# Kernel optimization log

Measured on AMD Instinct MI355X. Metric: run time of the kernel, lower is better.

Reference implementation:

```python
import jax, jax.numpy as jnp
import numpy as np

B, S, T, H, E, V, PAD = 128, 400, 50, 512, 128, 50000, 1000


def setup_inputs() -> dict:
    key = jax.random.key(0)
    ks = jax.random.split(key, 20)
    inp = {
        "input_token": jax.random.randint(ks[0], (B, 1), 0, V),
        "prev_decoder_h_states": jax.random.normal(ks[1], (B, T, H), jnp.float32),
        "last_hidden": jax.random.normal(ks[2], (B, H), jnp.float32),
        "encoder_states": jax.random.normal(ks[3], (B, S, H), jnp.float32),
        "full_input_var": jax.random.randint(ks[4], (B, S), 0, V + PAD),
        "previous_att": jax.random.normal(ks[5], (B, T, S), jnp.float32),
        "control_var": jax.random.normal(ks[6], (B, 1), jnp.float32),
        # learned parameters
        "emb": jax.random.normal(ks[7], (V, E), jnp.float32) * 0.02,
        "W_ih": jax.random.normal(ks[8], (3 * H, E), jnp.float32) * 0.05,
        "W_hh": jax.random.normal(ks[9], (3 * H, H), jnp.float32) * 0.05,
        "b_ih": jnp.zeros((3 * H,), jnp.float32),
        "b_hh": jnp.zeros((3 * H,), jnp.float32),
        "w_h": jax.random.normal(ks[10], (H,), jnp.float32) * 0.05,
        "w_d": jax.random.normal(ks[11], (H,), jnp.float32) * 0.05,
        "gen_W": jax.random.normal(ks[12], (1, 3 * H + 1), jnp.float32) * 0.05,
        "gen_b": jnp.zeros((1,), jnp.float32),
        "outh_W": jax.random.normal(ks[13], (E, 3 * H + 1), jnp.float32) * 0.05,
        "outh_b": jnp.zeros((E,), jnp.float32),
        "outv_W": jax.random.normal(ks[14], (V, E), jnp.float32) * 0.02,
        "outv_b": jnp.zeros((V,), jnp.float32),
    }
    return inp


def reference(input_token, prev_decoder_h_states, last_hidden, encoder_states,
              full_input_var, previous_att, control_var,
              emb, W_ih, W_hh, b_ih, b_hh, w_h, w_d,
              gen_W, gen_b, outh_W, outh_b, outv_W, outv_b):
    # embedding lookup (dropout = eval-mode identity); seq len is 1
    x = emb[input_token[:, 0]]                              # [B,E]
    # single GRU step (torch gate order: r, z, n)
    gx = x @ W_ih.T + b_ih                                  # [B,3H]
    gh = last_hidden @ W_hh.T + b_hh                        # [B,3H]
    r = jax.nn.sigmoid(gx[:, :H] + gh[:, :H])
    z = jax.nn.sigmoid(gx[:, H:2 * H] + gh[:, H:2 * H])
    n = jnp.tanh(gx[:, 2 * H:] + r * gh[:, 2 * H:])
    h = (1.0 - z) * n + z * last_hidden                     # decoder_hidden [B,H]

    # temporal encoder attention (previous_att is not None branch)
    att_scores = jnp.einsum("bh,bsh->bs", h, w_h[None, None, :] * encoder_states)
    temporal = jnp.exp(att_scores) / jnp.exp(previous_att).sum(1)   # [B,S]
    new_previous_att = jnp.concatenate([previous_att, att_scores[:, None, :]], axis=1)
    att_dist = temporal / temporal.sum(-1, keepdims=True)           # [B,S]

    # intra-decoder attention
    dec_scores = jnp.einsum("bh,bth->bt", h, w_d[None, None, :] * prev_decoder_h_states)
    dec_att = jax.nn.softmax(dec_scores, axis=-1)                   # [B,T]
    decoder_context = jnp.einsum("bt,bth->bh", dec_att, prev_decoder_h_states)

    encoder_context = jnp.einsum("bs,bsh->bh", att_dist, encoder_states)
    combined = jnp.concatenate([h, encoder_context, decoder_context, control_var], axis=-1)  # [B,3H+1]

    p_vocab = jax.nn.softmax((combined @ outh_W.T + outh_b) @ outv_W.T + outv_b, axis=-1)    # [B,V]
    p_gen = jax.nn.sigmoid(combined @ gen_W.T + gen_b)                                       # [B,1]

    # copy distribution via scatter-add over extended vocab V+PAD
    token_input_dist = jnp.zeros((input_token.shape[0], V + PAD), p_vocab.dtype)
    rows = jnp.arange(input_token.shape[0])[:, None]
    token_input_dist = token_input_dist.at[rows, full_input_var].add(att_dist)

    p_final = jnp.pad(p_vocab * p_gen, ((0, 0), (0, PAD))) + (1.0 - p_gen) * token_input_dist
    decoder_h_states = jnp.concatenate([prev_decoder_h_states, h[:, None, :]], axis=1)
    return (p_final, p_gen, p_vocab, att_dist, decoder_h_states, h, new_previous_att)
```

## Files before the change

kernel.cpp:

```cpp
#include <hip/hip_runtime.h>
#include <hip/hip_bf16.h>
#include <math.h>

constexpr int B = 128, S = 400, T = 50, H = 512, E = 128, V = 50000, PADV = 1000;
constexpr int NV = V + PADV;
constexpr int TH1 = 3 * H + 1;
constexpr int NBLK = 391;

constexpr int O_PFINAL = 0;
constexpr int O_PGEN   = O_PFINAL + B * NV;
constexpr int O_PVOCAB = O_PGEN + B;
constexpr int O_ATT    = O_PVOCAB + B * V;
constexpr int O_DHS    = O_ATT + B * S;
constexpr int O_H      = O_DHS + B * (T + 1) * H;
constexpr int O_NPA    = O_H + B * H;

constexpr int W_X    = 0;
constexpr int W_GX   = W_X + B * E;
constexpr int W_GH   = W_GX + B * 3 * H;
constexpr int W_HW   = W_GH + B * 3 * H;
constexpr int W_HD   = W_HW + B * H;
constexpr int W_SC   = W_HD + B * H;
constexpr int W_DEN  = W_SC + B * S;
constexpr int W_CMB  = W_DEN + B * S;
constexpr int W_LE   = W_CMB + B * TH1;
constexpr int W_RMAX = W_LE + B * E;
constexpr int W_RSUM = W_RMAX + B;
constexpr int W_PM   = W_RSUM + B;
constexpr int W_PS   = W_PM + B * NBLK;

__device__ __forceinline__ float wave_sum(float v) {
#pragma unroll
  for (int o = 32; o > 0; o >>= 1) v += __shfl_xor(v, o);
  return v;
}

__global__ void k_init(const int* __restrict__ tok, const float* __restrict__ emb,
                       const float* __restrict__ ctrl, float* __restrict__ ws) {
  int i = blockIdx.x * 256 + threadIdx.x;
  if (i < B * E) {
    int b = i >> 7, e = i & 127;
    ws[W_X + i] = emb[tok[b] * E + e];
  }
  if (i < B * H) {
    int b = i >> 9, h = i & 511;
    ws[W_CMB + b * TH1 + H + h] = 0.f;
  }
  if (i < B) ws[W_CMB + i * TH1 + 3 * H] = ctrl[i];
#pragma unroll
  for (int j = 0; j < 3; ++j) ws[W_GH + i + j * 65536] = 0.f;
}

__global__ __launch_bounds__(256) void k_grugemm(
    const float* __restrict__ x, const float* __restrict__ lh,
    const float* __restrict__ Wih, const float* __restrict__ Whh,
    float* __restrict__ ws) {
  __shared__ float As[32][132];
  __shared__ float Ws[32][36];
  const int tid = threadIdx.x;
  const int n0 = blockIdx.x * 32;
  const int y = blockIdx.y;
  const bool g0 = (y == 0);
  const float* A = g0 ? x : lh;
  const float* W = g0 ? Wih : Whh;
  const int K = g0 ? E : H;
  const int kbase = g0 ? 0 : (y - 1) * 128;
  const int tc = tid & 15;
  const int tr = tid >> 4;
  float acc[8][2] = {};
  for (int c = 0; c < 4; ++c) {
    const int k0 = kbase + c * 32;
    {
      int i = tid;
#pragma unroll
      for (int it = 0; it < 4; ++it, i += 256) {
        int b = i >> 3, k4 = i & 7;
        float4 v = *(const float4*)&A[b * K + k0 + k4 * 4];
        As[k4 * 4 + 0][b] = v.x; As[k4 * 4 + 1][b] = v.y;
        As[k4 * 4 + 2][b] = v.z; As[k4 * 4 + 3][b] = v.w;
      }
    }
    {
      int n = tid >> 3, k4 = tid & 7;
      float4 v = *(const float4*)&W[(n0 + n) * K + k0 + k4 * 4];
      Ws[k4 * 4 + 0][n] = v.x; Ws[k4 * 4 + 1][n] = v.y;
      Ws[k4 * 4 + 2][n] = v.z; Ws[k4 * 4 + 3][n] = v.w;
    }
    __syncthreads();
#pragma unroll
    for (int kk = 0; kk < 32; ++kk) {
      float4 a0 = *(const float4*)&As[kk][tr * 8];
      float4 a1 = *(const float4*)&As[kk][tr * 8 + 4];
      float2 w = *(const float2*)&Ws[kk][tc * 2];
      float av[8] = {a0.x, a0.y, a0.z, a0.w, a1.x, a1.y, a1.z, a1.w};
#pragma unroll
      for (int i = 0; i < 8; ++i) {
        acc[i][0] += av[i] * w.x;
        acc[i][1] += av[i] * w.y;
      }
    }
    __syncthreads();
  }
  if (g0) {
#pragma unroll
    for (int i = 0; i < 8; ++i) {
      float* dst = ws + W_GX + (tr * 8 + i) * (3 * H) + n0 + tc * 2;
      dst[0] = acc[i][0]; dst[1] = acc[i][1];
    }
  } else {
#pragma unroll
    for (int i = 0; i < 8; ++i) {
      float* dst = ws + W_GH + (tr * 8 + i) * (3 * H) + n0 + tc * 2;
      atomicAdd(dst, acc[i][0]); atomicAdd(dst + 1, acc[i][1]);
    }
  }
}

__global__ void k_gates(const float* __restrict__ ws_in, const float* __restrict__ lh,
                        const float* __restrict__ bih, const float* __restrict__ bhh,
                        const float* __restrict__ w_h, const float* __restrict__ w_d,
                        float* __restrict__ ws, float* __restrict__ out) {
  int i = blockIdx.x * 256 + threadIdx.x;
  int b = i >> 9, u = i & 511;
  const float* gx = ws_in + W_GX + b * (3 * H);
  const float* gh = ws_in + W_GH + b * (3 * H);
  float gxr = gx[u] + bih[u], gxz = gx[H + u] + bih[H + u], gxn = gx[2 * H + u] + bih[2 * H + u];
  float ghr = gh[u] + bhh[u], ghz = gh[H + u] + bhh[H + u], ghn = gh[2 * H + u] + bhh[2 * H + u];
  float r = 1.f / (1.f + __expf(-(gxr + ghr)));
  float z = 1.f / (1.f + __expf(-(gxz + ghz)));
  float n = tanhf(gxn + r * ghn);
  float lhv = lh[i];
  float h = (1.f - z) * n + z * lhv;
  out[O_H + i] = h;
  out[O_DHS + b * ((T + 1) * H) + T * H + u] = h;
  ws[W_CMB + b * TH1 + u] = h;
  ws[W_HW + i] = h * w_h[u];
  ws[W_HD + i] = h * w_d[u];
}

__global__ void k_den(const float* __restrict__ pa, float* __restrict__ ws,
                      float* __restrict__ out) {
  int i = blockIdx.x * 256 + threadIdx.x;
  if (i >= B * S) return;
  int b = i / S, s = i - b * S;
  float acc = 0.f;
  for (int t = 0; t < T; ++t) {
    float v = pa[(b * T + t) * S + s];
    out[O_NPA + (b * (T + 1) + t) * S + s] = v;
    acc += __expf(v);
  }
  ws[W_DEN + i] = acc;
}

__global__ void k_escore(const float* __restrict__ enc, float* __restrict__ ws,
                         float* __restrict__ out) {
  int blk = blockIdx.x;
  int b = blk / 25, sgrp = blk % 25;
  int wave = threadIdx.x >> 6, lane = threadIdx.x & 63;
  const float4* hw4 = (const float4*)(ws + W_HW + b * H);
  float4 h0 = hw4[lane * 2], h1 = hw4[lane * 2 + 1];
#pragma unroll
  for (int ii = 0; ii < 4; ++ii) {
    int s = sgrp * 16 + wave * 4 + ii;
    const float4* e4 = (const float4*)(enc + (b * S + s) * H);
    float4 e0 = e4[lane * 2], e1 = e4[lane * 2 + 1];
    float d = h0.x * e0.x + h0.y * e0.y + h0.z * e0.z + h0.w * e0.w +
              h1.x * e1.x + h1.y * e1.y + h1.z * e1.z + h1.w * e1.w;
    d = wave_sum(d);
    if (lane == 0) {
      ws[W_SC + b * S + s] = d;
      out[O_NPA + (b * (T + 1) + T) * S + s] = d;
    }
  }
}

__global__ void k_attdist(const float* __restrict__ ws, float* __restrict__ out) {
  int b = blockIdx.x, tid = threadIdx.x;
  __shared__ float red[4];
  int s0 = tid, s1 = tid + 256;
  float t0 = __expf(ws[W_SC + b * S + s0]) / ws[W_DEN + b * S + s0];
  float t1 = 0.f;
  if (s1 < S) t1 = __expf(ws[W_SC + b * S + s1]) / ws[W_DEN + b * S + s1];
  float loc = wave_sum(t0 + t1);
  if ((tid & 63) == 0) red[tid >> 6] = loc;
  __syncthreads();
  float inv = 1.f / (red[0] + red[1] + red[2] + red[3]);
  out[O_ATT + b * S + s0] = t0 * inv;
  if (s1 < S) out[O_ATT + b * S + s1] = t1 * inv;
}

__global__ void k_dec(const float* __restrict__ pd, float* __restrict__ ws,
                      float* __restrict__ out) {
  int b = blockIdx.x, tid = threadIdx.x;
  int wave = tid >> 6, lane = tid & 63;
  __shared__ float sc[T];
  const float4* hd4 = (const float4*)(ws + W_HD + b * H);
  float4 d0 = hd4[lane * 2], d1 = hd4[lane * 2 + 1];
  for (int t = wave; t < T; t += 4) {
    const float4* p4 = (const float4*)(pd + (b * T + t) * H);
    float4 p0 = p4[lane * 2], p1 = p4[lane * 2 + 1];
    float v = d0.x * p0.x + d0.y * p0.y + d0.z * p0.z + d0.w * p0.w +
              d1.x * p1.x + d1.y * p1.y + d1.z * p1.z + d1.w * p1.w;
    v = wave_sum(v);
    if (lane == 0) sc[t] = v;
  }
  __syncthreads();
  if (tid < 64) {
    float v = (lane < T) ? sc[lane] : -1e30f;
    float m = v;
#pragma unroll
    for (int o = 32; o > 0; o >>= 1) m = fmaxf(m, __shfl_xor(m, o));
    float e = (lane < T) ? __expf(v - m) : 0.f;
    float ssum = wave_sum(e);
    if (lane < T) sc[lane] = e / ssum;
  }
  __syncthreads();
  float a0 = 0.f, a1 = 0.f;
  int h0 = tid, h1 = tid + 256;
  for (int t = 0; t < T; ++t) {
    float wt = sc[t];
    a0 += wt * pd[(b * T + t) * H + h0];
    a1 += wt * pd[(b * T + t) * H + h1];
  }
  ws[W_CMB + b * TH1 + 2 * H + h0] = a0;
  ws[W_CMB + b * TH1 + 2 * H + h1] = a1;
}

__global__ void k_dhscopy(const float* __restrict__ pd, float* __restrict__ out) {
  int i = blockIdx.x * 256 + threadIdx.x;
  if (i >= B * T * H / 4) return;
  int b = i / (T * H / 4), rem = i - b * (T * H / 4);
  ((float4*)(out + O_DHS + b * (T + 1) * H))[rem] = ((const float4*)(pd + b * T * H))[rem];
}

__global__ void k_encctx(const float* __restrict__ enc, const float* __restrict__ out,
                         float* __restrict__ ws) {
  int blk = blockIdx.x;
  int b = blk / 5, c = blk % 5;
  int s0 = c * 80, tid = threadIdx.x;
  __shared__ float ad[80];
  if (tid < 80) ad[tid] = out[O_ATT + b * S + s0 + tid];
  __syncthreads();
  float a0 = 0.f, a1 = 0.f;
  int h0 = tid, h1 = tid + 256;
  for (int j = 0; j < 80; ++j) {
    float w = ad[j];
    const float* ep = enc + (b * S + s0 + j) * H;
    a0 += w * ep[h0];
    a1 += w * ep[h1];
  }
  atomicAdd(&ws[W_CMB + b * TH1 + H + h0], a0);
  atomicAdd(&ws[W_CMB + b * TH1 + H + h1], a1);
}

__global__ __launch_bounds__(256) void k_outh2(const float* __restrict__ oW,
                                               const float* __restrict__ ob,
                                               float* __restrict__ ws) {
  __shared__ float cmb[8 * TH1];
  const int tid = threadIdx.x;
  const int b0 = blockIdx.y * 8;
  const int e = blockIdx.x * 4 + (tid >> 6);
  const int lane = tid & 63;
  const float* src = ws + W_CMB + b0 * TH1;
  for (int i = tid; i < 8 * TH1; i += 256) cmb[i] = src[i];
  float wr[25];
  const float* wrow = oW + e * TH1;
#pragma unroll
  for (int j = 0; j < 25; ++j) {
    int k = lane + 64 * j;
    wr[j] = (k < TH1) ? wrow[k] : 0.f;
  }
  __syncthreads();
  float bias = ob[e];
#pragma unroll 1
  for (int bb = 0; bb < 8; ++bb) {
    const float* c = cmb + bb * TH1;
    float a = 0.f;
#pragma unroll
    for (int j = 0; j < 25; ++j) {
      int k = lane + 64 * j;
      float cv = (k < TH1) ? c[k] : 0.f;
      a += wr[j] * cv;
    }
    a = wave_sum(a);
    if (lane == 0) ws[W_LE + (b0 + bb) * E + e] = a + bias;
  }
}

__global__ void k_gen(const float* __restrict__ gW, const float* __restrict__ gb,
                      const float* __restrict__ ws, float* __restrict__ out) {
  int b = blockIdx.x, lane = threadIdx.x;
  float acc = 0.f;
  for (int k = lane; k < TH1; k += 64) acc += gW[k] * ws[W_CMB + b * TH1 + k];
  acc = wave_sum(acc);
  if (lane == 0) out[O_PGEN + b] = 1.f / (1.f + __expf(-(acc + gb[0])));
}

__global__ __launch_bounds__(256) void k_vgemm(
    const float* __restrict__ A, const float* __restrict__ W,
    const float* __restrict__ bias, float* __restrict__ C,
    float* __restrict__ ws) {
  __shared__ float As[32][132];
  __shared__ float Bs[32][132];
  const int tid = threadIdx.x;
  const int n0 = blockIdx.x * 128;
  const int tr = tid >> 4;
  const int tc = tid & 15;
  float acc[8][8] = {};
#pragma unroll 1
  for (int c = 0; c < 4; ++c) {
    const int k0 = c * 32;
    {
      int i = tid;
#pragma unroll
      for (int it = 0; it < 4; ++it, i += 256) {
        int m = i >> 3, k4 = i & 7;
        float4 v = *(const float4*)&A[m * 128 + k0 + k4 * 4];
        As[k4 * 4 + 0][m] = v.x; As[k4 * 4 + 1][m] = v.y;
        As[k4 * 4 + 2][m] = v.z; As[k4 * 4 + 3][m] = v.w;
      }
    }
    {
      int i = tid;
#pragma unroll
      for (int it = 0; it < 4; ++it, i += 256) {
        int n = i >> 3, k4 = i & 7;
        float4 v = make_float4(0.f, 0.f, 0.f, 0.f);
        if (n0 + n < V) v = *(const float4*)&W[(n0 + n) * 128 + k0 + k4 * 4];
        Bs[k4 * 4 + 0][n] = v.x; Bs[k4 * 4 + 1][n] = v.y;
        Bs[k4 * 4 + 2][n] = v.z; Bs[k4 * 4 + 3][n] = v.w;
      }
    }
    __syncthreads();
#pragma unroll 4
    for (int kk = 0; kk < 32; ++kk) {
      float4 a0 = *(const float4*)&As[kk][tr * 8];
      float4 a1 = *(const float4*)&As[kk][tr * 8 + 4];
      float4 b0 = *(const float4*)&Bs[kk][tc * 8];
      float4 b1 = *(const float4*)&Bs[kk][tc * 8 + 4];
      float av[8] = {a0.x, a0.y, a0.z, a0.w, a1.x, a1.y, a1.z, a1.w};
      float bw[8] = {b0.x, b0.y, b0.z, b0.w, b1.x, b1.y, b1.z, b1.w};
#pragma unroll
      for (int i = 0; i < 8; ++i)
#pragma unroll
        for (int j = 0; j < 8; ++j) acc[i][j] += av[i] * bw[j];
    }
    __syncthreads();
  }
  const int cbase = n0 + tc * 8;
  float bv[8];
#pragma unroll
  for (int j = 0; j < 8; ++j) bv[j] = (cbase + j < V) ? bias[cbase + j] : 0.f;
#pragma unroll
  for (int i = 0; i < 8; ++i) {
    int r = tr * 8 + i;
    float m = -1e30f;
#pragma unroll
    for (int j = 0; j < 8; ++j) {
      acc[i][j] += bv[j];
      if (cbase + j < V) m = fmaxf(m, acc[i][j]);
    }
#pragma unroll
    for (int o = 1; o < 16; o <<= 1) m = fmaxf(m, __shfl_xor(m, o));
    float s = 0.f;
#pragma unroll
    for (int j = 0; j < 8; ++j)
      if (cbase + j < V) s += __expf(acc[i][j] - m);
#pragma unroll
    for (int o = 1; o < 16; o <<= 1) s += __shfl_xor(s, o);
    if (tc == 0) {
      ws[W_PM + r * NBLK + blockIdx.x] = m;
      ws[W_PS + r * NBLK + blockIdx.x] = s;
    }
    if (cbase + 8 <= V) {
      *(float4*)&C[r * V + cbase] = make_float4(acc[i][0], acc[i][1], acc[i][2], acc[i][3]);
      *(float4*)&C[r * V + cbase + 4] = make_float4(acc[i][4], acc[i][5], acc[i][6], acc[i][7]);
    } else {
#pragma unroll
      for (int j = 0; j < 8; ++j)
        if (cbase + j < V) C[r * V + cbase + j] = acc[i][j];
    }
  }
}

__global__ void k_rowstat2(float* __restrict__ ws) {
  int b = blockIdx.x, tid = threadIdx.x;
  const float* pm = ws + W_PM + b * NBLK;
  const float* psv = ws + W_PS + b * NBLK;
  __shared__ float red[4];
  float m = -1e30f;
  for (int c = tid; c < NBLK; c += 256) m = fmaxf(m, pm[c]);
#pragma unroll
  for (int o = 32; o > 0; o >>= 1) m = fmaxf(m, __shfl_xor(m, o));
  if ((tid & 63) == 0) red[tid >> 6] = m;
  __syncthreads();
  float M = fmaxf(fmaxf(red[0], red[1]), fmaxf(red[2], red[3]));
  __syncthreads();
  float s = 0.f;
  for (int c = tid; c < NBLK; c += 256) s += psv[c] * __expf(pm[c] - M);
  s = wave_sum(s);
  if ((tid & 63) == 0) red[tid >> 6] = s;
  __syncthreads();
  if (tid == 0) {
    ws[W_RMAX + b] = M;
    ws[W_RSUM + b] = red[0] + red[1] + red[2] + red[3];
  }
}

__global__ void k_pvocab(const float* __restrict__ ws, float* __restrict__ out) {
  int b = blockIdx.y;
  int i = blockIdx.x * 256 + threadIdx.x;
  if (i >= V / 4) return;
  float m = ws[W_RMAX + b], inv = 1.f / ws[W_RSUM + b];
  float pg = out[O_PGEN + b];
  float4 v = ((const float4*)(out + O_PVOCAB + b * V))[i];
  float4 p;
  p.x = __expf(v.x - m) * inv;
  p.y = __expf(v.y - m) * inv;
  p.z = __expf(v.z - m) * inv;
  p.w = __expf(v.w - m) * inv;
  ((float4*)(out + O_PVOCAB + b * V))[i] = p;
  float4 pf;
  pf.x = pg * p.x; pf.y = pg * p.y; pf.z = pg * p.z; pf.w = pg * p.w;
  ((float4*)(out + O_PFINAL + b * NV))[i] = pf;
}

__global__ void k_pad(float* __restrict__ out) {
  int i = blockIdx.x * 256 + threadIdx.x;
  if (i >= B * PADV / 4) return;
  int b = i / (PADV / 4), j = i % (PADV / 4);
  ((float4*)(out + O_PFINAL + b * NV + V))[j] = make_float4(0.f, 0.f, 0.f, 0.f);
}

__global__ void k_scatter(const int* __restrict__ fiv, float* __restrict__ out) {
  int i = blockIdx.x * 256 + threadIdx.x;
  if (i >= B * S) return;
  int b = i / S;
  int idx = fiv[i];
  float pg = out[O_PGEN + b];
  float val = (1.f - pg) * out[O_ATT + i];
  atomicAdd(out + O_PFINAL + b * NV + idx, val);
}

extern "C" void kernel_launch(void* const* d_in, const int* in_sizes, int n_in,
                              void* d_out, int out_size, void* d_ws, size_t ws_size,
                              hipStream_t stream) {
  const int*   tok  = (const int*)d_in[0];
  const float* pd   = (const float*)d_in[1];
  const float* lh   = (const float*)d_in[2];
  const float* enc  = (const float*)d_in[3];
  const int*   fiv  = (const int*)d_in[4];
  const float* pa   = (const float*)d_in[5];
  const float* ctrl = (const float*)d_in[6];
  const float* emb  = (const float*)d_in[7];
  const float* W_ih = (const float*)d_in[8];
  const float* W_hh = (const float*)d_in[9];
  const float* b_ih = (const float*)d_in[10];
  const float* b_hh = (const float*)d_in[11];
  const float* w_h  = (const float*)d_in[12];
  const float* w_d  = (const float*)d_in[13];
  const float* gW   = (const float*)d_in[14];
  const float* gb   = (const float*)d_in[15];
  const float* ohW  = (const float*)d_in[16];
  const float* ohb  = (const float*)d_in[17];
  const float* ovW  = (const float*)d_in[18];
  const float* ovb  = (const float*)d_in[19];
  float* out = (float*)d_out;
  float* ws  = (float*)d_ws;

  k_init<<<256, 256, 0, stream>>>(tok, emb, ctrl, ws);
  k_grugemm<<<dim3(48, 5), 256, 0, stream>>>(ws + W_X, lh, W_ih, W_hh, ws);
  k_gates<<<256, 256, 0, stream>>>(ws, lh, b_ih, b_hh, w_h, w_d, ws, out);
  k_den<<<200, 256, 0, stream>>>(pa, ws, out);
  k_escore<<<3200, 256, 0, stream>>>(enc, ws, out);
  k_attdist<<<128, 256, 0, stream>>>(ws, out);
  k_dec<<<128, 256, 0, stream>>>(pd, ws, out);
  k_dhscopy<<<3200, 256, 0, stream>>>(pd, out);
  k_encctx<<<640, 256, 0, stream>>>(enc, out, ws);
  k_outh2<<<dim3(32, 16), 256, 0, stream>>>(ohW, ohb, ws);
  k_gen<<<128, 64, 0, stream>>>(gW, gb, ws, out);
  k_vgemm<<<NBLK, 256, 0, stream>>>(ws + W_LE, ovW, ovb, out + O_PVOCAB, ws);
  k_rowstat2<<<128, 256, 0, stream>>>(ws);
  k_pvocab<<<dim3(49, 128), 256, 0, stream>>>(ws, out);
  k_pad<<<125, 256, 0, stream>>>(out);
  k_scatter<<<200, 256, 0, stream>>>(fiv, out);
}
```

Before: 386.7 us.

## Fuse encoder context into score kernel and fold pad zeroing into pvocab

The encoder-score kernel now also computes the unnormalised attention weights exp(score)/den and accumulates a weighted sum of the encoder rows it already holds in registers. It also accumulates the per-batch weight total, both through atomics. This removes the separate k_encctx pass that re-read the whole 26 MB encoder tensor. The attdist kernel then normalises both the attention and the context by the accumulated total. Pad zeroing moves into k_pvocab as an extra grid column, dropping one launch. The cost is more atomic traffic and a change in float summation order.

```diff
diff --git a/kernel.cpp b/kernel.cpp
--- a/kernel.cpp
+++ b/kernel.cpp
@@ -28,6 +28,8 @@
 constexpr int W_RSUM = W_RMAX + B;
 constexpr int W_PM   = W_RSUM + B;
 constexpr int W_PS   = W_PM + B * NBLK;
+constexpr int W_ECX  = W_PS + B * NBLK;
+constexpr int W_TS   = W_ECX + B * H;
 
 __device__ __forceinline__ float wave_sum(float v) {
 #pragma unroll
@@ -42,11 +44,11 @@
     int b = i >> 7, e = i & 127;
     ws[W_X + i] = emb[tok[b] * E + e];
   }
-  if (i < B * H) {
-    int b = i >> 9, h = i & 511;
-    ws[W_CMB + b * TH1 + H + h] = 0.f;
-  }
-  if (i < B) ws[W_CMB + i * TH1 + 3 * H] = ctrl[i];
+  ws[W_ECX + i] = 0.f;
+  if (i < B) {
+    ws[W_TS + i] = 0.f;
+    ws[W_CMB + i * TH1 + 3 * H] = ctrl[i];
+  }
 #pragma unroll
   for (int j = 0; j < 3; ++j) ws[W_GH + i + j * 65536] = 0.f;
 }
@@ -154,11 +156,16 @@
 
 __global__ void k_escore(const float* __restrict__ enc, float* __restrict__ ws,
                          float* __restrict__ out) {
+  __shared__ float ctx[4][512];
+  __shared__ float tsw[4];
   int blk = blockIdx.x;
   int b = blk / 25, sgrp = blk % 25;
-  int wave = threadIdx.x >> 6, lane = threadIdx.x & 63;
+  int tid = threadIdx.x;
+  int wave = tid >> 6, lane = tid & 63;
   const float4* hw4 = (const float4*)(ws + W_HW + b * H);
   float4 h0 = hw4[lane * 2], h1 = hw4[lane * 2 + 1];
+  float c0[4] = {}, c1[4] = {};
+  float tsum = 0.f;
 #pragma unroll
   for (int ii = 0; ii < 4; ++ii) {
     int s = sgrp * 16 + wave * 4 + ii;
@@ -167,26 +174,35 @@
     float d = h0.x * e0.x + h0.y * e0.y + h0.z * e0.z + h0.w * e0.w +
               h1.x * e1.x + h1.y * e1.y + h1.z * e1.z + h1.w * e1.w;
     d = wave_sum(d);
+    float tmp = __expf(d) / ws[W_DEN + b * S + s];
     if (lane == 0) {
-      ws[W_SC + b * S + s] = d;
+      ws[W_SC + b * S + s] = tmp;
       out[O_NPA + (b * (T + 1) + T) * S + s] = d;
     }
-  }
-}
-
-__global__ void k_attdist(const float* __restrict__ ws, float* __restrict__ out) {
+    tsum += tmp;
+    c0[0] += tmp * e0.x; c0[1] += tmp * e0.y; c0[2] += tmp * e0.z; c0[3] += tmp * e0.w;
+    c1[0] += tmp * e1.x; c1[1] += tmp * e1.y; c1[2] += tmp * e1.z; c1[3] += tmp * e1.w;
+  }
+  *(float4*)&ctx[wave][lane * 8]     = make_float4(c0[0], c0[1], c0[2], c0[3]);
+  *(float4*)&ctx[wave][lane * 8 + 4] = make_float4(c1[0], c1[1], c1[2], c1[3]);
+  if (lane == 0) tsw[wave] = tsum;
+  __syncthreads();
+  for (int h = tid; h < H; h += 256) {
+    float v = ctx[0][h] + ctx[1][h] + ctx[2][h] + ctx[3][h];
+    atomicAdd(&ws[W_ECX + b * H + h], v);
+  }
+  if (tid == 0) atomicAdd(&ws[W_TS + b], tsw[0] + tsw[1] + tsw[2] + tsw[3]);
+}
+
+__global__ void k_attdist(const float* __restrict__ ws_in, float* __restrict__ ws,
+                          float* __restrict__ out) {
   int b = blockIdx.x, tid = threadIdx.x;
-  __shared__ float red[4];
+  float inv = 1.f / ws_in[W_TS + b];
   int s0 = tid, s1 = tid + 256;
-  float t0 = __expf(ws[W_SC + b * S + s0]) / ws[W_DEN + b * S + s0];
-  float t1 = 0.f;
-  if (s1 < S) t1 = __expf(ws[W_SC + b * S + s1]) / ws[W_DEN + b * S + s1];
-  float loc = wave_sum(t0 + t1);
-  if ((tid & 63) == 0) red[tid >> 6] = loc;
-  __syncthreads();
-  float inv = 1.f / (red[0] + red[1] + red[2] + red[3]);
-  out[O_ATT + b * S + s0] = t0 * inv;
-  if (s1 < S) out[O_ATT + b * S + s1] = t1 * inv;
+  out[O_ATT + b * S + s0] = ws_in[W_SC + b * S + s0] * inv;
+  if (s1 < S) out[O_ATT + b * S + s1] = ws_in[W_SC + b * S + s1] * inv;
+  for (int h = tid; h < H; h += 256)
+    ws[W_CMB + b * TH1 + H + h] = ws_in[W_ECX + b * H + h] * inv;
 }
 
 __global__ void k_dec(const float* __restrict__ pd, float* __restrict__ ws,
@@ -231,26 +247,6 @@
   if (i >= B * T * H / 4) return;
   int b = i / (T * H / 4), rem = i - b * (T * H / 4);
   ((float4*)(out + O_DHS + b * (T + 1) * H))[rem] = ((const float4*)(pd + b * T * H))[rem];
-}
-
-__global__ void k_encctx(const float* __restrict__ enc, const float* __restrict__ out,
-                         float* __restrict__ ws) {
-  int blk = blockIdx.x;
-  int b = blk / 5, c = blk % 5;
-  int s0 = c * 80, tid = threadIdx.x;
-  __shared__ float ad[80];
-  if (tid < 80) ad[tid] = out[O_ATT + b * S + s0 + tid];
-  __syncthreads();
-  float a0 = 0.f, a1 = 0.f;
-  int h0 = tid, h1 = tid + 256;
-  for (int j = 0; j < 80; ++j) {
-    float w = ad[j];
-    const float* ep = enc + (b * S + s0 + j) * H;
-    a0 += w * ep[h0];
-    a1 += w * ep[h1];
-  }
-  atomicAdd(&ws[W_CMB + b * TH1 + H + h0], a0);
-  atomicAdd(&ws[W_CMB + b * TH1 + H + h1], a1);
 }
 
 __global__ __launch_bounds__(256) void k_outh2(const float* __restrict__ oW,
@@ -410,7 +406,11 @@
 __global__ void k_pvocab(const float* __restrict__ ws, float* __restrict__ out) {
   int b = blockIdx.y;
   int i = blockIdx.x * 256 + threadIdx.x;
-  if (i >= V / 4) return;
+  if (i >= NV / 4) return;
+  if (i >= V / 4) {
+    ((float4*)(out + O_PFINAL + b * NV))[i] = make_float4(0.f, 0.f, 0.f, 0.f);
+    return;
+  }
   float m = ws[W_RMAX + b], inv = 1.f / ws[W_RSUM + b];
   float pg = out[O_PGEN + b];
   float4 v = ((const float4*)(out + O_PVOCAB + b * V))[i];
@@ -423,13 +423,6 @@
   float4 pf;
   pf.x = pg * p.x; pf.y = pg * p.y; pf.z = pg * p.z; pf.w = pg * p.w;
   ((float4*)(out + O_PFINAL + b * NV))[i] = pf;
-}
-
-__global__ void k_pad(float* __restrict__ out) {
-  int i = blockIdx.x * 256 + threadIdx.x;
-  if (i >= B * PADV / 4) return;
-  int b = i / (PADV / 4), j = i % (PADV / 4);
-  ((float4*)(out + O_PFINAL + b * NV + V))[j] = make_float4(0.f, 0.f, 0.f, 0.f);
 }
 
 __global__ void k_scatter(const int* __restrict__ fiv, float* __restrict__ out) {
@@ -473,15 +466,13 @@
   k_gates<<<256, 256, 0, stream>>>(ws, lh, b_ih, b_hh, w_h, w_d, ws, out);
   k_den<<<200, 256, 0, stream>>>(pa, ws, out);
   k_escore<<<3200, 256, 0, stream>>>(enc, ws, out);
-  k_attdist<<<128, 256, 0, stream>>>(ws, out);
+  k_attdist<<<128, 256, 0, stream>>>(ws, ws, out);
   k_dec<<<128, 256, 0, stream>>>(pd, ws, out);
   k_dhscopy<<<3200, 256, 0, stream>>>(pd, out);
-  k_encctx<<<640, 256, 0, stream>>>(enc, out, ws);
   k_outh2<<<dim3(32, 16), 256, 0, stream>>>(ohW, ohb, ws);
   k_gen<<<128, 64, 0, stream>>>(gW, gb, ws, out);
   k_vgemm<<<NBLK, 256, 0, stream>>>(ws + W_LE, ovW, ovb, out + O_PVOCAB, ws);
   k_rowstat2<<<128, 256, 0, stream>>>(ws);
-  k_pvocab<<<dim3(49, 128), 256, 0, stream>>>(ws, out);
-  k_pad<<<125, 256, 0, stream>>>(out);
+  k_pvocab<<<dim3(50, 128), 256, 0, stream>>>(ws, out);
   k_scatter<<<200, 256, 0, stream>>>(fiv, out);
 }
```

Measured after the change: 372.4 us. 3.7% less time.
